# Kernel tuning notes

Measured on AMD Instinct MI355X. Metric: run time of the kernel, lower is better.

The kernel has to match this reference:

```python
import jax, jax.numpy as jnp
import numpy as np

N_HEAD = 8


def setup_inputs() -> dict:
    key = jax.random.key(0)
    ks = jax.random.split(key, 4)
    B, L, C = 4, 1024, 512
    x = jax.random.normal(ks[0], (B, L, C), dtype=jnp.float32)
    adj = jax.random.uniform(ks[1], (B, L, L), dtype=jnp.float32)
    W_qkv = jax.random.normal(ks[2], (3 * C, C), dtype=jnp.float32) * 0.02
    W_proj = jax.random.normal(ks[3], (C, C), dtype=jnp.float32) * 0.02
    bias_scale = jnp.array([3.0, 3.0], dtype=jnp.float32)
    beta = jnp.ones((3,), dtype=jnp.float32) / 3.0
    return {"x": x, "adj": adj, "W_qkv": W_qkv, "W_proj": W_proj,
            "bias_scale": bias_scale, "beta": beta}


def _branch_attn(Q, K, V, scale, bias=None):
    # Q,K,V: [B,H,L,D]
    S = jnp.einsum('bhqd,bhkd->bhqk', Q, K) / scale
    if bias is not None:
        S = S + bias
    attn = jax.nn.softmax(S, axis=-1)
    return jnp.einsum('bhqk,bhkd->bhqd', attn, V)


def reference(x, adj, W_qkv, W_proj, bias_scale, beta):
    B, L, C = x.shape
    H = N_HEAD
    D = C // H
    scale = jnp.sqrt(jnp.float32(D))

    qkv = x @ W_qkv.T  # [B,L,3C]
    Q, K, V = jnp.split(qkv, 3, axis=-1)
    Q = Q.reshape(B, L, H, D).transpose(0, 2, 1, 3)  # [B,H,L,D]
    K = K.reshape(B, L, H, D).transpose(0, 2, 1, 3)
    V = V.reshape(B, L, H, D).transpose(0, 2, 1, 3)

    # has_cls: zero out CLS row/col in adjacency
    adj_local = adj.at[:, 0, :].set(0.0).at[:, :, 0].set(0.0)
    B_fwd = adj_local[:, None, :, :]              # [B,1,L,L]
    B_bwd = jnp.swapaxes(adj_local, -1, -2)[:, None, :, :]

    h0 = _branch_attn(Q, K, V, scale)
    h1 = _branch_attn(Q, K, V, scale, bias_scale[0] * B_fwd)
    h2 = _branch_attn(Q, K, V, scale, bias_scale[1] * B_bwd)

    b = jax.nn.softmax(beta, axis=0)
    out = b[0] * h0 + b[1] * h1 + b[2] * h2      # [B,H,L,D]
    out = out.transpose(0, 2, 1, 3).reshape(B, L, C)
    return out @ W_proj.T
```

## Files before the change

kernel.cpp:

```cpp
#include <hip/hip_runtime.h>
#include <hip/hip_bf16.h>
#include <stdint.h>

#define B_  4
#define L_  1024
#define C_  512
#define H_  8
#define D_  64
#define BH_ 32
#define M_  4096

typedef short  bf16x8 __attribute__((ext_vector_type(8)));
typedef float  f32x4  __attribute__((ext_vector_type(4)));
typedef unsigned short u16x8 __attribute__((ext_vector_type(8)));
typedef unsigned int   u32x2 __attribute__((ext_vector_type(2)));

__device__ __forceinline__ unsigned short f2bf(float f) {
    union { float f; uint32_t u; } v; v.f = f;
    uint32_t u = v.u;
    return (unsigned short)((u + 0x7fffu + ((u >> 16) & 1u)) >> 16);
}
__device__ __forceinline__ float bf2f(unsigned short s) {
    union { uint32_t u; float f; } v; v.u = ((uint32_t)s) << 16;
    return v.f;
}

__device__ __forceinline__ void gload16(const void* g, void* s) {
    __builtin_amdgcn_global_load_lds((const __attribute__((address_space(1))) void*)g,
                                     (__attribute__((address_space(3))) void*)s, 16, 0, 0);
}

#define NX4   (M_ * C_ / 4)
#define NWQ4  (3 * C_ * C_ / 4)
#define NWP4  (C_ * C_ / 4)
__global__ void cvt_all(const float* __restrict__ x, const float* __restrict__ wq,
                        const float* __restrict__ wp,
                        unsigned short* __restrict__ xb, unsigned short* __restrict__ wqb,
                        unsigned short* __restrict__ wpb) {
    int i = blockIdx.x * 256 + threadIdx.x;
    const float* src; unsigned short* dst; int o;
    if (i < NX4) { src = x; dst = xb; o = i; }
    else if (i < NX4 + NWQ4) { src = wq; dst = wqb; o = i - NX4; }
    else if (i < NX4 + NWQ4 + NWP4) { src = wp; dst = wpb; o = i - NX4 - NWQ4; }
    else return;
    float4 v = ((const float4*)src)[o];
    ushort4 r;
    r.x = f2bf(v.x); r.y = f2bf(v.y); r.z = f2bf(v.z); r.w = f2bf(v.w);
    ((ushort4*)dst)[o] = r;
}

__global__ __launch_bounds__(256) void prep_e(const float* __restrict__ adj,
                                              const float* __restrict__ bias_scale,
                                              unsigned short* __restrict__ EI) {
    __shared__ float Tr[64][65];
    const int b = blockIdx.z, q0 = blockIdx.y * 64, k0 = blockIdx.x * 64;
    const float* adjb = adj + (size_t)b * L_ * L_;
    const int tid = threadIdx.x;
#pragma unroll
    for (int i = 0; i < 4; ++i) {
        int idx = i * 256 + tid;
        int rk = idx >> 4, c4 = (idx & 15) * 4;
        float4 v = *(const float4*)(adjb + (size_t)(k0 + rk) * L_ + q0 + c4);
        Tr[rk][c4 + 0] = v.x; Tr[rk][c4 + 1] = v.y; Tr[rk][c4 + 2] = v.z; Tr[rk][c4 + 3] = v.w;
    }
    __syncthreads();
    const float bs0 = bias_scale[0], bs1 = bias_scale[1];
    const int w = tid >> 6, l = tid & 63, g = l >> 4, c = l & 15;
#pragma unroll
    for (int qs = 0; qs < 4; ++qs) {
        int ql = qs * 16 + c, qg = q0 + ql;
        int klb = w * 16 + g * 4;
        float4 af4 = *(const float4*)(adjb + (size_t)qg * L_ + k0 + klb);
        unsigned short ef[4], eb[4];
        const float afv[4] = {af4.x, af4.y, af4.z, af4.w};
#pragma unroll
        for (int i = 0; i < 4; ++i) {
            int kg = k0 + klb + i;
            bool z = (qg == 0) || (kg == 0);
            ef[i] = f2bf(z ? 1.0f : __expf(bs0 * afv[i]));
            eb[i] = f2bf(z ? 1.0f : __expf(bs1 * Tr[klb + i][ql]));
        }
        size_t o = (((size_t)b * 64 + (blockIdx.y * 4 + qs)) * 64 + (blockIdx.x * 4 + w)) * 512 + (size_t)l * 8;
        u16x8 o8 = {ef[0], ef[1], ef[2], ef[3], eb[0], eb[1], eb[2], eb[3]};
        *(u16x8*)(EI + o) = o8;
    }
}

template <int BM, int BN, int KDIM, int EPI, int NDIM>
__global__ __launch_bounds__(256, 4) void gemm_bf16(const unsigned short* __restrict__ Amat,
                                                    const unsigned short* __restrict__ Bmat,
                                                    float* __restrict__ outp,
                                                    unsigned short* __restrict__ q_out,
                                                    unsigned short* __restrict__ k_out,
                                                    unsigned short* __restrict__ v_out) {
    constexpr int NA = BM / 32, NB = BN / 32;
    constexpr int MI = BM / 32, NI = BN / 32;
    __shared__ __align__(16) unsigned short As[BM * 64];
    __shared__ __align__(16) unsigned short Bs[BN * 64];
    const int tid = threadIdx.x;
    const int l = tid & 63, wid = tid >> 6;
    const int g = l >> 4, c = l & 15;
    const int wr = wid >> 1, wc = wid & 1;
    const int row0 = blockIdx.y * BM, col0 = blockIdx.x * BN;

    f32x4 acc[MI][NI];
#pragma unroll
    for (int mi = 0; mi < MI; ++mi)
#pragma unroll
        for (int ni = 0; ni < NI; ++ni) acc[mi][ni] = (f32x4){0.f, 0.f, 0.f, 0.f};

    for (int k0 = 0; k0 < KDIM; k0 += 64) {
        bf16x8 ra[NA], rb[NB];
#pragma unroll
        for (int i = 0; i < NA; ++i) {
            int q = i * 256 + tid;
            int r = q >> 3, cb = (q & 7) * 16;
            ra[i] = *(const bf16x8*)((const char*)Amat + (size_t)(row0 + r) * (KDIM * 2) + k0 * 2 + cb);
        }
#pragma unroll
        for (int i = 0; i < NB; ++i) {
            int q = i * 256 + tid;
            int r = q >> 3, cb = (q & 7) * 16;
            rb[i] = *(const bf16x8*)((const char*)Bmat + (size_t)(col0 + r) * (KDIM * 2) + k0 * 2 + cb);
        }
        __syncthreads();
#pragma unroll
        for (int i = 0; i < NA; ++i) {
            int q = i * 256 + tid;
            int r = q >> 3, cb = (q & 7) * 16;
            *(bf16x8*)((char*)As + r * 128 + (cb ^ ((r & 7) << 4))) = ra[i];
        }
#pragma unroll
        for (int i = 0; i < NB; ++i) {
            int q = i * 256 + tid;
            int r = q >> 3, cb = (q & 7) * 16;
            *(bf16x8*)((char*)Bs + r * 128 + (cb ^ ((r & 7) << 4))) = rb[i];
        }
        __syncthreads();
#pragma unroll
        for (int kk = 0; kk < 2; ++kk) {
            bf16x8 afr[MI], bfr[NI];
#pragma unroll
            for (int mi = 0; mi < MI; ++mi) {
                int r = wr * (BM / 2) + mi * 16 + c;
                afr[mi] = *(const bf16x8*)((const char*)As + r * 128 + ((kk * 64 + g * 16) ^ ((r & 7) << 4)));
            }
#pragma unroll
            for (int ni = 0; ni < NI; ++ni) {
                int r = wc * (BN / 2) + ni * 16 + c;
                bfr[ni] = *(const bf16x8*)((const char*)Bs + r * 128 + ((kk * 64 + g * 16) ^ ((r & 7) << 4)));
            }
#pragma unroll
            for (int mi = 0; mi < MI; ++mi)
#pragma unroll
                for (int ni = 0; ni < NI; ++ni)
                    acc[mi][ni] = __builtin_amdgcn_mfma_f32_16x16x32_bf16(afr[mi], bfr[ni], acc[mi][ni], 0, 0, 0);
        }
    }
#pragma unroll
    for (int mi = 0; mi < MI; ++mi) {
#pragma unroll
        for (int ni = 0; ni < NI; ++ni) {
#pragma unroll
            for (int ii = 0; ii < 4; ++ii) {
                int m = row0 + wr * (BM / 2) + mi * 16 + g * 4 + ii;
                int n = col0 + wc * (BN / 2) + ni * 16 + c;
                float val = acc[mi][ni][ii];
                if (EPI == 0) {
                    unsigned short v = f2bf(val);
                    int b = m >> 10, ll = m & 1023;
                    int which = n >> 9, cc = n & 511;
                    int hh = cc >> 6, d = cc & 63;
                    int bh = b * 8 + hh;
                    if (which == 0)      q_out[((size_t)bh * L_ + ll) * D_ + d] = v;
                    else if (which == 1) k_out[((size_t)bh * L_ + ll) * D_ + d] = v;
                    else                 v_out[((size_t)bh * D_ + d) * L_ + ll] = v;
                } else {
                    outp[(size_t)m * NDIM + n] = val;
                }
            }
        }
    }
}

struct EReg { bf16x8 e[4]; };

__global__ __launch_bounds__(256, 2) void attn_kernel(const unsigned short* __restrict__ Qb,
                                                      const unsigned short* __restrict__ Kb,
                                                      const unsigned short* __restrict__ Vtb,
                                                      const unsigned short* __restrict__ EI,
                                                      const float* __restrict__ beta,
                                                      unsigned short* __restrict__ hb) {
    __shared__ __align__(16) char smem[2][16384];
    const int tid = threadIdx.x;
    const int w = tid >> 6, l = tid & 63;
    const int g = l >> 4, c = l & 15;

    const int p = blockIdx.x;
    const int s = (p & 7) + 8 * (p >> 6);
    const int h = (p >> 3) & 7;
    const int b = s >> 4, qb = s & 15;
    const int bh = b * 8 + h;
    const int q0 = qb * 64 + w * 16;
    const int qt = qb * 4 + w;

    const unsigned short* Qrow = Qb + ((size_t)bh * L_ + q0 + c) * D_;
    const bf16x8 qf0 = *(const bf16x8*)(Qrow + g * 8);
    const bf16x8 qf1 = *(const bf16x8*)(Qrow + 32 + g * 8);

    const unsigned short* Kbase = Kb + (size_t)bh * L_ * D_;
    const unsigned short* Vbase = Vtb + (size_t)bh * D_ * L_;
    const unsigned short* Ebase = EI + ((size_t)(b * 64 + qt) * 64) * 512;

    f32x4 O[3][4];
#pragma unroll
    for (int j = 0; j < 3; ++j)
#pragma unroll
        for (int dc = 0; dc < 4; ++dc) O[j][dc] = (f32x4){0.f, 0.f, 0.f, 0.f};
    float lsum0 = 0.f, lsum1 = 0.f, lsum2 = 0.f;

    const int srow = l >> 3, sm = l & 7;
    const int key = (c & 7) << 4;

    auto stage = [&](int t, char* base) {
#pragma unroll
        for (int n = 0; n < 2; ++n) {
            int i = 2 * w + n;
            int row = i * 8 + srow;
            int sw = (sm ^ (row & 7)) * 8;
            gload16(Kbase + (size_t)(t * 64 + row) * D_ + sw, base + i * 1024);
            gload16(Vbase + (size_t)row * L_ + t * 64 + sw, base + 8192 + i * 1024);
        }
    };
    auto eload = [&](EReg& X, int t) {
#pragma unroll
        for (int ks = 0; ks < 4; ++ks)
            X.e[ks] = *(const bf16x8*)(Ebase + (size_t)(t * 4 + ks) * 512 + l * 8);
    };

    auto compute = [&](const char* base, const EReg& E) {
        const char* Kl = base;
        const char* Vl = base + 8192;
        unsigned r[4][3][2];
#pragma unroll
        for (int st = 0; st < 4; ++st) {
            const char* kr = Kl + (st * 16 + c) * 128;
            bf16x8 ka = *(const bf16x8*)(kr + ((g * 16) ^ key));
            bf16x8 kb = *(const bf16x8*)(kr + ((64 + g * 16) ^ key));
            f32x4 sacc = (f32x4){0.f, 0.f, 0.f, 0.f};
            sacc = __builtin_amdgcn_mfma_f32_16x16x32_bf16(ka, qf0, sacc, 0, 0, 0);
            sacc = __builtin_amdgcn_mfma_f32_16x16x32_bf16(kb, qf1, sacc, 0, 0, 0);
            float pv[3][4];
#pragma unroll
            for (int i = 0; i < 4; ++i) {
                float p0 = __expf(sacc[i] * 0.125f);
                float p1 = p0 * bf2f((unsigned short)E.e[st][i]);
                float p2 = p0 * bf2f((unsigned short)E.e[st][4 + i]);
                lsum0 += p0; lsum1 += p1; lsum2 += p2;
                pv[0][i] = p0; pv[1][i] = p1; pv[2][i] = p2;
            }
#pragma unroll
            for (int j = 0; j < 3; ++j) {
                r[st][j][0] = __builtin_amdgcn_perm(__float_as_uint(pv[j][1]), __float_as_uint(pv[j][0]), 0x07060302u);
                r[st][j][1] = __builtin_amdgcn_perm(__float_as_uint(pv[j][3]), __float_as_uint(pv[j][2]), 0x07060302u);
            }
        }
#pragma unroll
        for (int kk = 0; kk < 2; ++kk) {
            bf16x8 af[3];
#pragma unroll
            for (int j = 0; j < 3; ++j) {
                union { unsigned u[4]; bf16x8 v; } t_;
                t_.u[0] = r[2 * kk][j][0];     t_.u[1] = r[2 * kk][j][1];
                t_.u[2] = r[2 * kk + 1][j][0]; t_.u[3] = r[2 * kk + 1][j][1];
                af[j] = t_.v;
            }
#pragma unroll
            for (int dc = 0; dc < 4; ++dc) {
                const char* vr = Vl + (dc * 16 + c) * 128;
                u32x2 vlo = *(const u32x2*)(vr + ((kk * 64 + g * 8) ^ key));
                u32x2 vhi = *(const u32x2*)(vr + ((kk * 64 + 32 + g * 8) ^ key));
                union { unsigned u[4]; bf16x8 v; } bv;
                bv.u[0] = vlo[0]; bv.u[1] = vlo[1]; bv.u[2] = vhi[0]; bv.u[3] = vhi[1];
#pragma unroll
                for (int j = 0; j < 3; ++j)
                    O[j][dc] = __builtin_amdgcn_mfma_f32_16x16x32_bf16(af[j], bv.v, O[j][dc], 0, 0, 0);
            }
        }
    };

    EReg E0, E1;
    stage(0, smem[0]);
    eload(E0, 0);
    __syncthreads();
#pragma unroll 1
    for (int t = 0; t < 16; t += 2) {
        stage(t + 1, smem[1]);
        eload(E1, t + 1);
        compute(smem[0], E0);
        __syncthreads();
        if (t + 2 < 16) { stage(t + 2, smem[0]); eload(E0, t + 2); }
        compute(smem[1], E1);
        __syncthreads();
    }

    lsum0 += __shfl_xor(lsum0, 16); lsum0 += __shfl_xor(lsum0, 32);
    lsum1 += __shfl_xor(lsum1, 16); lsum1 += __shfl_xor(lsum1, 32);
    lsum2 += __shfl_xor(lsum2, 16); lsum2 += __shfl_xor(lsum2, 32);

    float b0 = beta[0], b1 = beta[1], b2 = beta[2];
    float bm = fmaxf(b0, fmaxf(b1, b2));
    float e0 = __expf(b0 - bm), e1 = __expf(b1 - bm), e2 = __expf(b2 - bm);
    float inv = 1.0f / (e0 + e1 + e2);
    float i0 = e0 * inv / lsum0, i1 = e1 * inv / lsum1, i2 = e2 * inv / lsum2;

    float iq0[4], iq1[4], iq2[4];
#pragma unroll
    for (int ii = 0; ii < 4; ++ii) {
        iq0[ii] = __shfl(i0, g * 4 + ii);
        iq1[ii] = __shfl(i1, g * 4 + ii);
        iq2[ii] = __shfl(i2, g * 4 + ii);
    }
    const int hcol = (bh & 7) * 64;
#pragma unroll
    for (int dc = 0; dc < 4; ++dc) {
#pragma unroll
        for (int ii = 0; ii < 4; ++ii) {
            float hv = iq0[ii] * O[0][dc][ii] + iq1[ii] * O[1][dc][ii] + iq2[ii] * O[2][dc][ii];
            int qrow = q0 + g * 4 + ii;
            hb[((size_t)(b << 10) + qrow) * C_ + hcol + dc * 16 + c] = f2bf(hv);
        }
    }
}

extern "C" void kernel_launch(void* const* d_in, const int* in_sizes, int n_in,
                              void* d_out, int out_size, void* d_ws, size_t ws_size,
                              hipStream_t stream) {
    const float* x          = (const float*)d_in[0];
    const float* adj        = (const float*)d_in[1];
    const float* wqkv       = (const float*)d_in[2];
    const float* wproj      = (const float*)d_in[3];
    const float* bias_scale = (const float*)d_in[4];
    const float* beta       = (const float*)d_in[5];
    float* out = (float*)d_out;

    char* ws = (char*)d_ws;
    size_t off = 0;
    auto alloc = [&](size_t bytes) {
        void* p = ws + off;
        off += (bytes + 255) & ~(size_t)255;
        return p;
    };
    unsigned short* xb     = (unsigned short*)alloc((size_t)M_ * C_ * 2);
    unsigned short* wqkvb  = (unsigned short*)alloc((size_t)3 * C_ * C_ * 2);
    unsigned short* wprojb = (unsigned short*)alloc((size_t)C_ * C_ * 2);
    unsigned short* Qb     = (unsigned short*)alloc((size_t)BH_ * L_ * D_ * 2);
    unsigned short* Kb     = (unsigned short*)alloc((size_t)BH_ * L_ * D_ * 2);
    unsigned short* Vtb    = (unsigned short*)alloc((size_t)BH_ * D_ * L_ * 2);
    unsigned short* EI     = (unsigned short*)alloc((size_t)B_ * L_ * L_ * 4);
    unsigned short* hb     = (unsigned short*)alloc((size_t)M_ * C_ * 2);

    cvt_all<<<(NX4 + NWQ4 + NWP4 + 255) / 256, 256, 0, stream>>>(x, wqkv, wproj, xb, wqkvb, wprojb);
    prep_e<<<dim3(L_ / 64, L_ / 64, B_), 256, 0, stream>>>(adj, bias_scale, EI);
    gemm_bf16<64, 128, 512, 0, 0><<<dim3(1536 / 128, M_ / 64), 256, 0, stream>>>(xb, wqkvb, nullptr, Qb, Kb, Vtb);
    attn_kernel<<<dim3(512), 256, 0, stream>>>(Qb, Kb, Vtb, EI, beta, hb);
    gemm_bf16<64, 64, 512, 1, 512><<<dim3(512 / 64, M_ / 64), 256, 0, stream>>>(hb, wprojb, out, nullptr, nullptr, nullptr);
}
```

Baseline: 71.84 us.

## Fuse adjacency exp-bias prep and QKV GEMM into one interleaved kernel

Merges the prep_e kernel (adjacency transpose and exp bias computation) and the QKV projection GEMM into a single launch. Block indices are interleaved so that every 7 consecutive blocks hold 3 GEMM tiles and 4 prep tiles. The aim is to overlap the memory-bound bias prep with the compute-bound GEMM and remove one kernel launch. The cost is a larger shared buffer and fewer waves per SIMD (launch bounds drop from 4 to 2), which could reduce occupancy for the GEMM part.

```diff
diff --git a/kernel.cpp b/kernel.cpp
--- a/kernel.cpp
+++ b/kernel.cpp
@@ -5,7 +5,6 @@
 #define B_  4
 #define L_  1024
 #define C_  512
-#define H_  8
 #define D_  64
 #define BH_ 32
 #define M_  4096
@@ -49,50 +48,141 @@
     ((ushort4*)dst)[o] = r;
 }
 
-__global__ __launch_bounds__(256) void prep_e(const float* __restrict__ adj,
-                                              const float* __restrict__ bias_scale,
-                                              unsigned short* __restrict__ EI) {
-    __shared__ float Tr[64][65];
-    const int b = blockIdx.z, q0 = blockIdx.y * 64, k0 = blockIdx.x * 64;
-    const float* adjb = adj + (size_t)b * L_ * L_;
-    const int tid = threadIdx.x;
-#pragma unroll
-    for (int i = 0; i < 4; ++i) {
-        int idx = i * 256 + tid;
-        int rk = idx >> 4, c4 = (idx & 15) * 4;
-        float4 v = *(const float4*)(adjb + (size_t)(k0 + rk) * L_ + q0 + c4);
-        Tr[rk][c4 + 0] = v.x; Tr[rk][c4 + 1] = v.y; Tr[rk][c4 + 2] = v.z; Tr[rk][c4 + 3] = v.w;
-    }
-    __syncthreads();
-    const float bs0 = bias_scale[0], bs1 = bias_scale[1];
-    const int w = tid >> 6, l = tid & 63, g = l >> 4, c = l & 15;
-#pragma unroll
-    for (int qs = 0; qs < 4; ++qs) {
-        int ql = qs * 16 + c, qg = q0 + ql;
-        int klb = w * 16 + g * 4;
-        float4 af4 = *(const float4*)(adjb + (size_t)qg * L_ + k0 + klb);
-        unsigned short ef[4], eb[4];
-        const float afv[4] = {af4.x, af4.y, af4.z, af4.w};
-#pragma unroll
-        for (int i = 0; i < 4; ++i) {
-            int kg = k0 + klb + i;
-            bool z = (qg == 0) || (kg == 0);
-            ef[i] = f2bf(z ? 1.0f : __expf(bs0 * afv[i]));
-            eb[i] = f2bf(z ? 1.0f : __expf(bs1 * Tr[klb + i][ql]));
-        }
-        size_t o = (((size_t)b * 64 + (blockIdx.y * 4 + qs)) * 64 + (blockIdx.x * 4 + w)) * 512 + (size_t)l * 8;
-        u16x8 o8 = {ef[0], ef[1], ef[2], ef[3], eb[0], eb[1], eb[2], eb[3]};
-        *(u16x8*)(EI + o) = o8;
-    }
-}
-
-template <int BM, int BN, int KDIM, int EPI, int NDIM>
-__global__ __launch_bounds__(256, 4) void gemm_bf16(const unsigned short* __restrict__ Amat,
+__global__ __launch_bounds__(256, 2) void fused_pre(const unsigned short* __restrict__ Amat,
                                                     const unsigned short* __restrict__ Bmat,
-                                                    float* __restrict__ outp,
                                                     unsigned short* __restrict__ q_out,
                                                     unsigned short* __restrict__ k_out,
-                                                    unsigned short* __restrict__ v_out) {
+                                                    unsigned short* __restrict__ v_out,
+                                                    const float* __restrict__ adj,
+                                                    const float* __restrict__ bias_scale,
+                                                    unsigned short* __restrict__ EI) {
+    __shared__ __align__(16) char sm[24576];
+    const int tid = threadIdx.x;
+    const int gb = blockIdx.x;
+    const int u = gb % 7, grp = gb / 7;
+
+    if (u < 3) {
+        const int tile = grp * 3 + u;
+        const int row0 = (tile / 12) * 64, col0 = (tile % 12) * 128;
+        unsigned short* As = (unsigned short*)sm;
+        unsigned short* Bs = (unsigned short*)(sm + 8192);
+        const int l = tid & 63, wid = tid >> 6;
+        const int g = l >> 4, c = l & 15;
+        const int wr = wid >> 1, wc = wid & 1;
+
+        f32x4 acc[2][4];
+#pragma unroll
+        for (int mi = 0; mi < 2; ++mi)
+#pragma unroll
+            for (int ni = 0; ni < 4; ++ni) acc[mi][ni] = (f32x4){0.f, 0.f, 0.f, 0.f};
+
+        for (int k0 = 0; k0 < 512; k0 += 64) {
+            bf16x8 ra[2], rb[4];
+#pragma unroll
+            for (int i = 0; i < 2; ++i) {
+                int q = i * 256 + tid;
+                int r = q >> 3, cb = (q & 7) * 16;
+                ra[i] = *(const bf16x8*)((const char*)Amat + (size_t)(row0 + r) * 1024 + k0 * 2 + cb);
+            }
+#pragma unroll
+            for (int i = 0; i < 4; ++i) {
+                int q = i * 256 + tid;
+                int r = q >> 3, cb = (q & 7) * 16;
+                rb[i] = *(const bf16x8*)((const char*)Bmat + (size_t)(col0 + r) * 1024 + k0 * 2 + cb);
+            }
+            __syncthreads();
+#pragma unroll
+            for (int i = 0; i < 2; ++i) {
+                int q = i * 256 + tid;
+                int r = q >> 3, cb = (q & 7) * 16;
+                *(bf16x8*)((char*)As + r * 128 + (cb ^ ((r & 7) << 4))) = ra[i];
+            }
+#pragma unroll
+            for (int i = 0; i < 4; ++i) {
+                int q = i * 256 + tid;
+                int r = q >> 3, cb = (q & 7) * 16;
+                *(bf16x8*)((char*)Bs + r * 128 + (cb ^ ((r & 7) << 4))) = rb[i];
+            }
+            __syncthreads();
+#pragma unroll
+            for (int kk = 0; kk < 2; ++kk) {
+                bf16x8 afr[2], bfr[4];
+#pragma unroll
+                for (int mi = 0; mi < 2; ++mi) {
+                    int r = wr * 32 + mi * 16 + c;
+                    afr[mi] = *(const bf16x8*)((const char*)As + r * 128 + ((kk * 64 + g * 16) ^ ((r & 7) << 4)));
+                }
+#pragma unroll
+                for (int ni = 0; ni < 4; ++ni) {
+                    int r = wc * 64 + ni * 16 + c;
+                    bfr[ni] = *(const bf16x8*)((const char*)Bs + r * 128 + ((kk * 64 + g * 16) ^ ((r & 7) << 4)));
+                }
+#pragma unroll
+                for (int mi = 0; mi < 2; ++mi)
+#pragma unroll
+                    for (int ni = 0; ni < 4; ++ni)
+                        acc[mi][ni] = __builtin_amdgcn_mfma_f32_16x16x32_bf16(afr[mi], bfr[ni], acc[mi][ni], 0, 0, 0);
+            }
+        }
+#pragma unroll
+        for (int mi = 0; mi < 2; ++mi) {
+#pragma unroll
+            for (int ni = 0; ni < 4; ++ni) {
+#pragma unroll
+                for (int ii = 0; ii < 4; ++ii) {
+                    int m = row0 + wr * 32 + mi * 16 + g * 4 + ii;
+                    int n = col0 + wc * 64 + ni * 16 + c;
+                    unsigned short v = f2bf(acc[mi][ni][ii]);
+                    int b = m >> 10, ll = m & 1023;
+                    int which = n >> 9, cc = n & 511;
+                    int hh = cc >> 6, d = cc & 63;
+                    int bh = b * 8 + hh;
+                    if (which == 0)      q_out[((size_t)bh * L_ + ll) * D_ + d] = v;
+                    else if (which == 1) k_out[((size_t)bh * L_ + ll) * D_ + d] = v;
+                    else                 v_out[((size_t)bh * D_ + d) * L_ + ll] = v;
+                }
+            }
+        }
+    } else {
+        const int pb = grp * 4 + (u - 3);
+        const int kx = pb & 15, qy = (pb >> 4) & 15, bz = pb >> 8;
+        const int q0 = qy * 64, k0 = kx * 64;
+        float (*Tr)[65] = (float(*)[65])sm;
+        const float* adjb = adj + (size_t)bz * L_ * L_;
+#pragma unroll
+        for (int i = 0; i < 4; ++i) {
+            int idx = i * 256 + tid;
+            int rk = idx >> 4, c4 = (idx & 15) * 4;
+            float4 v = *(const float4*)(adjb + (size_t)(k0 + rk) * L_ + q0 + c4);
+            Tr[rk][c4 + 0] = v.x; Tr[rk][c4 + 1] = v.y; Tr[rk][c4 + 2] = v.z; Tr[rk][c4 + 3] = v.w;
+        }
+        __syncthreads();
+        const float bs0 = bias_scale[0], bs1 = bias_scale[1];
+        const int w = tid >> 6, l = tid & 63, g = l >> 4, c = l & 15;
+#pragma unroll
+        for (int qs = 0; qs < 4; ++qs) {
+            int ql = qs * 16 + c, qg = q0 + ql;
+            int klb = w * 16 + g * 4;
+            float4 af4 = *(const float4*)(adjb + (size_t)qg * L_ + k0 + klb);
+            unsigned short ef[4], eb[4];
+            const float afv[4] = {af4.x, af4.y, af4.z, af4.w};
+#pragma unroll
+            for (int e = 0; e < 4; ++e) {
+                int kg = k0 + klb + e;
+                bool z = (qg == 0) || (kg == 0);
+                ef[e] = f2bf(z ? 1.0f : __expf(bs0 * afv[e]));
+                eb[e] = f2bf(z ? 1.0f : __expf(bs1 * Tr[klb + e][ql]));
+            }
+            size_t o = (((size_t)bz * 64 + (qy * 4 + qs)) * 64 + (kx * 4 + w)) * 512 + (size_t)l * 8;
+            *(u16x8*)(EI + o) = (u16x8){ef[0], ef[1], ef[2], ef[3], eb[0], eb[1], eb[2], eb[3]};
+        }
+    }
+}
+
+template <int BM, int BN, int KDIM, int NDIM>
+__global__ __launch_bounds__(256, 4) void gemm_proj(const unsigned short* __restrict__ Amat,
+                                                    const unsigned short* __restrict__ Bmat,
+                                                    float* __restrict__ outp) {
     constexpr int NA = BM / 32, NB = BN / 32;
     constexpr int MI = BM / 32, NI = BN / 32;
     __shared__ __align__(16) unsigned short As[BM * 64];
@@ -158,29 +248,15 @@
         }
     }
 #pragma unroll
-    for (int mi = 0; mi < MI; ++mi) {
-#pragma unroll
-        for (int ni = 0; ni < NI; ++ni) {
+    for (int mi = 0; mi < MI; ++mi)
+#pragma unroll
+        for (int ni = 0; ni < NI; ++ni)
 #pragma unroll
             for (int ii = 0; ii < 4; ++ii) {
                 int m = row0 + wr * (BM / 2) + mi * 16 + g * 4 + ii;
                 int n = col0 + wc * (BN / 2) + ni * 16 + c;
-                float val = acc[mi][ni][ii];
-                if (EPI == 0) {
-                    unsigned short v = f2bf(val);
-                    int b = m >> 10, ll = m & 1023;
-                    int which = n >> 9, cc = n & 511;
-                    int hh = cc >> 6, d = cc & 63;
-                    int bh = b * 8 + hh;
-                    if (which == 0)      q_out[((size_t)bh * L_ + ll) * D_ + d] = v;
-                    else if (which == 1) k_out[((size_t)bh * L_ + ll) * D_ + d] = v;
-                    else                 v_out[((size_t)bh * D_ + d) * L_ + ll] = v;
-                } else {
-                    outp[(size_t)m * NDIM + n] = val;
-                }
-            }
-        }
-    }
+                outp[(size_t)m * NDIM + n] = acc[mi][ni][ii];
+            }
 }
 
 struct EReg { bf16x8 e[4]; };
@@ -241,7 +317,7 @@
     auto compute = [&](const char* base, const EReg& E) {
         const char* Kl = base;
         const char* Vl = base + 8192;
-        unsigned r[4][3][2];
+        unsigned rr[4][3][2];
 #pragma unroll
         for (int st = 0; st < 4; ++st) {
             const char* kr = Kl + (st * 16 + c) * 128;
@@ -261,8 +337,8 @@
             }
 #pragma unroll
             for (int j = 0; j < 3; ++j) {
-                r[st][j][0] = __builtin_amdgcn_perm(__float_as_uint(pv[j][1]), __float_as_uint(pv[j][0]), 0x07060302u);
-                r[st][j][1] = __builtin_amdgcn_perm(__float_as_uint(pv[j][3]), __float_as_uint(pv[j][2]), 0x07060302u);
+                rr[st][j][0] = __builtin_amdgcn_perm(__float_as_uint(pv[j][1]), __float_as_uint(pv[j][0]), 0x07060302u);
+                rr[st][j][1] = __builtin_amdgcn_perm(__float_as_uint(pv[j][3]), __float_as_uint(pv[j][2]), 0x07060302u);
             }
         }
 #pragma unroll
@@ -271,8 +347,8 @@
 #pragma unroll
             for (int j = 0; j < 3; ++j) {
                 union { unsigned u[4]; bf16x8 v; } t_;
-                t_.u[0] = r[2 * kk][j][0];     t_.u[1] = r[2 * kk][j][1];
-                t_.u[2] = r[2 * kk + 1][j][0]; t_.u[3] = r[2 * kk + 1][j][1];
+                t_.u[0] = rr[2 * kk][j][0];     t_.u[1] = rr[2 * kk][j][1];
+                t_.u[2] = rr[2 * kk + 1][j][0]; t_.u[3] = rr[2 * kk + 1][j][1];
                 af[j] = t_.v;
             }
 #pragma unroll
@@ -361,8 +437,7 @@
     unsigned short* hb     = (unsigned short*)alloc((size_t)M_ * C_ * 2);
 
     cvt_all<<<(NX4 + NWQ4 + NWP4 + 255) / 256, 256, 0, stream>>>(x, wqkv, wproj, xb, wqkvb, wprojb);
-    prep_e<<<dim3(L_ / 64, L_ / 64, B_), 256, 0, stream>>>(adj, bias_scale, EI);
-    gemm_bf16<64, 128, 512, 0, 0><<<dim3(1536 / 128, M_ / 64), 256, 0, stream>>>(xb, wqkvb, nullptr, Qb, Kb, Vtb);
+    fused_pre<<<dim3(1792), 256, 0, stream>>>(xb, wqkvb, Qb, Kb, Vtb, adj, bias_scale, EI);
     attn_kernel<<<dim3(512), 256, 0, stream>>>(Qb, Kb, Vtb, EI, beta, hb);
-    gemm_bf16<64, 64, 512, 1, 512><<<dim3(512 / 64, M_ / 64), 256, 0, stream>>>(hb, wprojb, out, nullptr, nullptr, nullptr);
-}
+    gemm_proj<64, 64, 512, 512><<<dim3(512 / 64, M_ / 64), 256, 0, stream>>>(hb, wprojb, out);
+}
```

New measurement: 76.97 us. +7.1%, slower.
